# Kernel tuning notes

Hardware: AMD Instinct MI355X
Metric: run time of the kernel (lower is better)

## Reference

```python
import jax, jax.numpy as jnp
import numpy as np

FEATURES = [3, 64, 128, 256]
N_ITER = 5  # NNMF multiplicative-update iterations
K = 3
PAD = K // 2  # 'same' padding so spatial dims are preserved inside a block
EPS = 1e-20
BN_EPS = 1e-5


def conv2d(x, w, pad):
    # x: [B, Cin, H, W], w: [Cout, Cin, kh, kw] (torch OIHW layout)
    return jax.lax.conv_general_dilated(
        x, w, window_strides=(1, 1),
        padding=[(pad, pad), (pad, pad)],
        dimension_numbers=("NCHW", "OIHW", "NCHW"))


def nnmf_conv2d(x, w, n_iter, pad):
    # Non-negative, L1-normalized weights (per output filter)
    wp = jnp.abs(w)
    wn = wp / (wp.sum(axis=(1, 2, 3), keepdims=True) + EPS)
    # Input is non-negative (ReLU applied upstream); L1-normalize over channels
    x = x / (x.sum(axis=1, keepdims=True) + EPS)
    b, _, hh, ww = x.shape
    c_out = w.shape[0]
    # h init: uniform distribution over output channels
    h = jnp.full((b, c_out, hh, ww), 1.0 / c_out, dtype=x.dtype)
    # conv_transpose2d(h, W, padding=pad) == conv2d(h, flip(W).swap(O,I), padding=k-1-pad);
    # with odd k and pad = k//2 this is again 'same' padding.
    wt = jnp.transpose(jnp.flip(wn, (2, 3)), (1, 0, 2, 3))  # [Cin, Cout, kh, kw] as OIHW
    for _ in range(n_iter):
        recon = conv2d(h, wt, pad)                    # [B, Cin, H, W]
        h = h * conv2d(x / (recon + EPS), wn, pad)    # multiplicative update
        h = h / (h.sum(axis=1, keepdims=True) + EPS)  # renormalize over channels
    return h


def batchnorm(x, gamma, beta):
    # Training-mode BN: batch statistics over (N, H, W), biased variance
    mean = x.mean(axis=(0, 2, 3), keepdims=True)
    var = x.var(axis=(0, 2, 3), keepdims=True)
    xn = (x - mean) * jax.lax.rsqrt(var + BN_EPS)
    return xn * gamma[None, :, None, None] + beta[None, :, None, None]


def avgpool2(x):
    b, c, h, w = x.shape
    return x.reshape(b, c, h // 2, 2, w // 2, 2).mean(axis=(3, 5))


def block(x, w_nnmf, w_conv, b_conv, gamma, beta):
    x = jax.nn.relu(x)
    h = nnmf_conv2d(x, w_nnmf, N_ITER, PAD)
    y = conv2d(h, w_conv, 0) + b_conv[None, :, None, None]  # 1x1 conv
    y = jax.nn.relu(y)
    y = batchnorm(y, gamma, beta)
    return avgpool2(y)


def setup_inputs() -> dict:
    key = jax.random.key(0)
    keys = jax.random.split(key, 7)
    inp = {"x": jax.random.normal(keys[0], (16, 3, 128, 128), jnp.float32)}
    for i in range(3):
        cin, cout = FEATURES[i], FEATURES[i + 1]
        inp[f"w_nnmf{i}"] = jax.random.uniform(keys[1 + 2 * i], (cout, cin, K, K), jnp.float32)
        inp[f"w_conv{i}"] = jax.random.normal(keys[2 + 2 * i], (cout, cout, 1, 1), jnp.float32) / np.sqrt(cout).astype(np.float32)
        inp[f"b_conv{i}"] = jnp.zeros((cout,), jnp.float32)
        inp[f"gamma{i}"] = jnp.ones((cout,), jnp.float32)
        inp[f"beta{i}"] = jnp.zeros((cout,), jnp.float32)
    return inp


def reference(x, w_nnmf0, w_conv0, b_conv0, gamma0, beta0,
              w_nnmf1, w_conv1, b_conv1, gamma1, beta1,
              w_nnmf2, w_conv2, b_conv2, gamma2, beta2):
    x = block(x, w_nnmf0, w_conv0, b_conv0, gamma0, beta0)
    x = block(x, w_nnmf1, w_conv1, b_conv1, gamma1, beta1)
    x = block(x, w_nnmf2, w_conv2, b_conv2, gamma2, beta2)
    return x  # [16, 256, 16, 16]
```

## Files before the change

kernel.cpp:

```cpp
#include <hip/hip_runtime.h>

#define EPSV  1e-20f
#define BNEPS 1e-5f

typedef _Float16 f16x8 __attribute__((ext_vector_type(8)));
typedef _Float16 f16x4 __attribute__((ext_vector_type(4)));
typedef float    f32x4 __attribute__((ext_vector_type(4)));

__device__ inline unsigned pack2f16(float a, float b) {
    unsigned short ua = __builtin_bit_cast(unsigned short, (_Float16)a);
    unsigned short ub = __builtin_bit_cast(unsigned short, (_Float16)b);
    return ((unsigned)ub << 16) | ua;
}

template<int CIN, int COUT>
__global__ __launch_bounds__(256) void prep_w_f16_kernel(const float* __restrict__ w,
                                                         _Float16* __restrict__ wAh,
                                                         _Float16* __restrict__ wBh)
{
    const int co  = blockIdx.x;
    const int tid = threadIdx.x;
    const int N   = CIN * 9;
    const float* wrow = w + (size_t)co * N;

    float s = 0.f;
    for (int i = tid; i < N; i += 256) s += fabsf(wrow[i]);
    __shared__ float red[4];
    #pragma unroll
    for (int m = 32; m; m >>= 1) s += __shfl_xor(s, m, 64);
    if ((tid & 63) == 0) red[tid >> 6] = s;
    __syncthreads();
    s = red[0] + red[1] + red[2] + red[3];
    const float rn = 1.f / (s + EPSV);

    for (int i = tid; i < N; i += 256) {
        const int ci = i / 9, tap = i % 9;
        const int ky = tap / 3, kx = tap % 3;
        const float v = fabsf(wrow[i]) * rn;
        const int tf = (2 - ky) * 3 + (2 - kx);
        wBh[(((size_t)(ci >> 5) * 9 + tap) * COUT + co) * 32 + (ci & 31)] = (_Float16)v;
        wAh[(((size_t)(co >> 5) * 9 + tf) * CIN + ci) * 32 + (co & 31)] = (_Float16)v;
    }
}

__global__ __launch_bounds__(256) void zero_f16_kernel(_Float16* __restrict__ a, int n)
{
    const int i = blockIdx.x * 256 + threadIdx.x;
    if (i < n) a[i] = (_Float16)0.f;
}

__global__ __launch_bounds__(64) void prep_w0_kernel(const float* __restrict__ w,
                                                     _Float16* __restrict__ wA0h,
                                                     _Float16* __restrict__ wB0h)
{
    const int co = blockIdx.x, tid = threadIdx.x;
    float s = (tid < 27) ? fabsf(w[co * 27 + tid]) : 0.f;
    #pragma unroll
    for (int m = 32; m; m >>= 1) s += __shfl_xor(s, m, 64);
    const float rn = 1.f / (s + EPSV);
    if (tid < 27) {
        const int ci = tid / 9, tap = tid % 9, ky = tap / 3, kx = tap % 3;
        const float v = fabsf(w[co * 27 + tid]) * rn;
        const int tf = (2 - ky) * 3 + (2 - kx);
        wB0h[co * 64 + tap * 4 + ci] = (_Float16)v;
        wA0h[(((co >> 5) * 9 + tf) * 16 + ci) * 32 + (co & 31)] = (_Float16)v;
    }
}

__global__ __launch_bounds__(256) void prep_w1h_kernel(const float* __restrict__ w1,
                                                       _Float16* __restrict__ w1h, int n)
{
    const int i = blockIdx.x * 256 + threadIdx.x;
    if (i < n) w1h[i] = (_Float16)w1[i];
}

__global__ __launch_bounds__(256) void xn0_kernel(const float* __restrict__ x,
                                                  _Float16* __restrict__ xn4,
                                                  int npx, int HW)
{
    const int p = blockIdx.x * 256 + threadIdx.x;
    if (p >= npx) return;
    const int b = p / HW, r = p % HW;
    const float* ip = x + (size_t)b * 3 * HW + r;
    const float v0 = fmaxf(ip[0], 0.f), v1 = fmaxf(ip[HW], 0.f), v2 = fmaxf(ip[2 * HW], 0.f);
    const float rs = 1.f / (v0 + v1 + v2 + EPSV);
    unsigned* d = (unsigned*)(xn4 + (size_t)p * 4);
    d[0] = pack2f16(v0 * rs, v1 * rs);
    d[1] = pack2f16(v2 * rs, 0.f);
}

template<int C>
__global__ __launch_bounds__(256) void xn12_kernel(const _Float16* __restrict__ prev,
                                                   _Float16* __restrict__ xn, int npx)
{
    const int p = blockIdx.x * 256 + threadIdx.x;
    if (p >= npx) return;
    const _Float16* ip = prev + (size_t)p * C;
    _Float16* op = xn + (size_t)p * C;
    f16x8 buf[C / 8];
    float s = 0.f;
    #pragma unroll
    for (int g = 0; g < C / 8; ++g) {
        buf[g] = *(const f16x8*)(ip + g * 8);
        #pragma unroll
        for (int j = 0; j < 8; ++j) {
            float v = fmaxf((float)buf[g][j], 0.f);
            s += v;
            buf[g][j] = (_Float16)v;
        }
    }
    const float rs = 1.f / (s + EPSV);
    #pragma unroll
    for (int g = 0; g < C / 8; ++g) {
        f16x8 o;
        #pragma unroll
        for (int j = 0; j < 8; ++j) o[j] = (_Float16)((float)buf[g][j] * rs);
        *(f16x8*)(op + g * 8) = o;
    }
}

__global__ __launch_bounds__(256) void init_h_kernel(_Float16* __restrict__ h, float* __restrict__ S,
                                                     int nh, int ns, float cval)
{
    const int i = blockIdx.x * 256 + threadIdx.x;
    if (i < nh) h[i] = (_Float16)1.f;
    if (i < ns) S[i] = cval;
}

template<int NS>
__global__ __launch_bounds__(256) void combine_S_kernel(const float* __restrict__ sp,
                                                        float* __restrict__ S, int npx)
{
    const int i = blockIdx.x * 256 + threadIdx.x;
    if (i >= npx) return;
    float s = sp[i];
    #pragma unroll
    for (int k = 1; k < NS; ++k) s += sp[(size_t)k * npx + i];
    S[i] = s;
}

template<int ICg, int OCg, int NSPLIT, int OST, int NW, bool NORM_IN, bool UPDATE>
__global__ __launch_bounds__(256, 1) void mfconv5(
    const _Float16* __restrict__ in, const _Float16* __restrict__ wgt,
    const _Float16* __restrict__ aux, _Float16* __restrict__ out,
    const float* __restrict__ Sin, float* __restrict__ Sout,
    int H, int W, int sstride)
{
    constexpr int OCWG = OCg / NSPLIT;
    constexpr int NF = OCWG / 16;
    constexpr int HS = 18, WSp = 18, NSP = HS * WSp;
    constexpr int ICP = 40;
    constexpr int NCH = ICg / 32;
    constexpr int LS = (NSPLIT == 4) ? 2 : (NSPLIT == 2) ? 1 : 0;
    constexpr int NLD = NSP * 4;
    constexpr int IREG = (NLD + 255) / 256;
    constexpr int WOC = OCWG * 32;
    constexpr int NWLD = 9 * OCWG * 4;
    constexpr int WREG = (NWLD + 255) / 256;
    static_assert(OCWG % 16 == 0 && ICg % 32 == 0, "cfg");

    __shared__ _Float16 in_t[2][NSP * ICP];
    __shared__ _Float16 w_t[2][9 * WOC];
    __shared__ float rS[NORM_IN ? NSP : 1];

    const int tid = threadIdx.x;
    const int lane = tid & 63, wave = tid >> 6;
    const int kq = lane >> 4, l15 = lane & 15;
    const int split = blockIdx.x & (NSPLIT - 1);
    const int tx = blockIdx.x >> LS;
    const int x0 = tx * 16, y0 = blockIdx.y * 16, b = blockIdx.z;
    const int HW = H * W;
    const int oc0 = split * OCWG;

    f16x8 ild[IREG];
    f16x8 wld[WREG];

    auto iload = [&](int kc) {
        #pragma unroll
        for (int r = 0; r < IREG; ++r) {
            const int i = tid + r * 256;
            f16x8 v = {0, 0, 0, 0, 0, 0, 0, 0};
            if (i < NLD) {
                const int sp = i >> 2, seg = i & 3;
                const int yy = y0 + sp / WSp - 1, xx = x0 + sp % WSp - 1;
                if (yy >= 0 && yy < H && xx >= 0 && xx < W)
                    v = __builtin_nontemporal_load((const f16x8*)(in +
                        ((size_t)b * HW + (size_t)yy * W + xx) * ICg + kc * 32 + seg * 8));
            }
            ild[r] = v;
        }
    };
    auto wload = [&](int kc) {
        #pragma unroll
        for (int r = 0; r < WREG; ++r) {
            const int j = tid + r * 256;
            if (j < NWLD) {
                const int tap = j / (OCWG * 4), rem = j % (OCWG * 4);
                const int oc = rem >> 2, e = rem & 3;
                wld[r] = *(const f16x8*)(wgt +
                    (((size_t)kc * 9 + tap) * OCg + oc0 + oc) * 32 + e * 8);
            }
        }
    };
    auto iwrite = [&](int buf) {
        #pragma unroll
        for (int r = 0; r < IREG; ++r) {
            const int i = tid + r * 256;
            if (i < NLD) {
                const int sp = i >> 2, seg = i & 3;
                if constexpr (NORM_IN) {
                    const float f = rS[sp];
                    unsigned* d = (unsigned*)&in_t[buf][sp * ICP + seg * 8];
                    d[0] = pack2f16((float)ild[r][0] * f, (float)ild[r][1] * f);
                    d[1] = pack2f16((float)ild[r][2] * f, (float)ild[r][3] * f);
                    d[2] = pack2f16((float)ild[r][4] * f, (float)ild[r][5] * f);
                    d[3] = pack2f16((float)ild[r][6] * f, (float)ild[r][7] * f);
                } else {
                    *(f16x8*)&in_t[buf][sp * ICP + seg * 8] = ild[r];
                }
            }
        }
    };
    auto wwrite = [&](int buf) {
        #pragma unroll
        for (int r = 0; r < WREG; ++r) {
            const int j = tid + r * 256;
            if (j < NWLD) {
                const int tap = j / (OCWG * 4), rem = j % (OCWG * 4);
                const int oc = rem >> 2, e = rem & 3;
                const int slot = e ^ ((oc >> 1) & 3);
                *(f16x8*)&w_t[buf][tap * WOC + oc * 32 + slot * 8] = wld[r];
            }
        }
    };

    const int prow = wave * 4;

    f32x4 acc[4][NF];
    #pragma unroll
    for (int mf = 0; mf < 4; ++mf)
        #pragma unroll
        for (int nf = 0; nf < NF; ++nf) acc[mf][nf] = (f32x4){0.f, 0.f, 0.f, 0.f};

    iload(0); wload(0);
    if constexpr (NORM_IN) {
        for (int i = tid; i < NSP; i += 256) {
            const int yy = y0 + i / WSp - 1, xx = x0 + i % WSp - 1;
            float sv = 0.f;
            if (yy >= 0 && yy < H && xx >= 0 && xx < W)
                sv = Sin[(size_t)b * HW + (size_t)yy * W + xx];
            rS[i] = 1.f / (sv + EPSV);
        }
        __syncthreads();
    }
    iwrite(0); wwrite(0);
    __syncthreads();

    int cur = 0;
    for (int kc = 0; kc < NCH; ++kc) {
        if (kc + 1 < NCH) { iload(kc + 1); wload(kc + 1); }
        {
            const _Float16* ib = &in_t[cur][0];
            const _Float16* wb = &w_t[cur][0];
            #pragma unroll
            for (int dy = 0; dy < 3; ++dy) {
                #pragma unroll
                for (int dx = 0; dx < 3; ++dx) {
                    const int tap = dy * 3 + dx;
                    f16x8 bfr[NF];
                    #pragma unroll
                    for (int nf = 0; nf < NF; ++nf) {
                        const int oc = nf * 16 + l15;
                        bfr[nf] = *(const f16x8*)(
                            wb + tap * WOC + oc * 32 + (kq ^ ((oc >> 1) & 3)) * 8);
                    }
                    f16x8 afr[4];
                    #pragma unroll
                    for (int mf = 0; mf < 4; ++mf)
                        afr[mf] = *(const f16x8*)(
                            ib + ((prow + mf + dy) * WSp + l15 + dx) * ICP + kq * 8);
                    #pragma unroll
                    for (int mf = 0; mf < 4; ++mf)
                        #pragma unroll
                        for (int nf = 0; nf < NF; ++nf)
                            acc[mf][nf] = __builtin_amdgcn_mfma_f32_16x16x32_f16(
                                afr[mf], bfr[nf], acc[mf][nf], 0, 0, 0);
                }
            }
        }
        if (kc + 1 < NCH) {
            iwrite(cur ^ 1); wwrite(cur ^ 1);
            __syncthreads();
            cur ^= 1;
        }
    }

    #pragma unroll
    for (int mf = 0; mf < 4; ++mf) {
        const int gy = y0 + prow + mf;
        const size_t pixbase = (size_t)b * HW + (size_t)gy * W + x0 + kq * 4;
        if constexpr (!UPDATE) {
            #pragma unroll
            for (int nf = 0; nf < NF; ++nf) {
                const int oc = oc0 + nf * 16 + l15;
                if (oc < NW) {
                    #pragma unroll
                    for (int r = 0; r < 4; ++r) {
                        const size_t idx = (pixbase + r) * OST + oc;
                        out[idx] = (_Float16)((float)aux[idx] / (acc[mf][nf][r] + EPSV));
                    }
                }
            }
        } else {
            float s[4] = {0.f, 0.f, 0.f, 0.f};
            #pragma unroll
            for (int nf = 0; nf < NF; ++nf) {
                const int oc = oc0 + nf * 16 + l15;
                #pragma unroll
                for (int r = 0; r < 4; ++r) {
                    const size_t idx = (pixbase + r) * OST + oc;
                    const float hv = (float)out[idx] * acc[mf][nf][r];
                    const _Float16 hq = (_Float16)hv;
                    out[idx] = hq;
                    s[r] += (float)hq;
                }
            }
            #pragma unroll
            for (int mm = 1; mm < 16; mm <<= 1) {
                #pragma unroll
                for (int r = 0; r < 4; ++r) s[r] += __shfl_xor(s[r], mm);
            }
            if (l15 == 0) {
                float* sp_ = Sout + (size_t)split * sstride + pixbase;
                sp_[0] = s[0]; sp_[1] = s[1]; sp_[2] = s[2]; sp_[3] = s[3];
            }
        }
    }
}

__global__ __launch_bounds__(256) void mf0u_kernel(
    const _Float16* __restrict__ ratio4, const _Float16* __restrict__ wB0h,
    _Float16* __restrict__ h, float* __restrict__ Sout, int H, int W)
{
    constexpr int TW = 16;
    __shared__ _Float16 a_t[64 * 72];

    const int tid = threadIdx.x;
    const int lane = tid & 63, wave = tid >> 6;
    const int kq = lane >> 4, l15 = lane & 15;
    const int x0 = blockIdx.x * TW, y0 = blockIdx.y * 4, b = blockIdx.z;
    const int HW = H * W;

    for (int i = tid; i < 64 * 72 / 2; i += 256) ((unsigned*)a_t)[i] = 0;
    __syncthreads();
    for (int i = tid; i < 576; i += 256) {
        const int px = i / 9, tap = i % 9;
        const int py = px / TW, pxx = px % TW;
        const int yy = y0 + py + tap / 3 - 1, xx = x0 + pxx + tap % 3 - 1;
        if (yy >= 0 && yy < H && xx >= 0 && xx < W)
            *(f16x4*)&a_t[px * 72 + tap * 4] =
                *(const f16x4*)(ratio4 + ((size_t)b * HW + (size_t)yy * W + xx) * 4);
    }
    __syncthreads();

    f32x4 acc[4];
    #pragma unroll
    for (int nf = 0; nf < 4; ++nf) acc[nf] = (f32x4){0.f, 0.f, 0.f, 0.f};
    #pragma unroll
    for (int kc = 0; kc < 2; ++kc) {
        const f16x8 afr = *(const f16x8*)&a_t[(wave * 16 + l15) * 72 + kc * 32 + kq * 8];
        #pragma unroll
        for (int nf = 0; nf < 4; ++nf) {
            const f16x8 bfr = *(const f16x8*)(wB0h + (size_t)(nf * 16 + l15) * 64 + kc * 32 + kq * 8);
            acc[nf] = __builtin_amdgcn_mfma_f32_16x16x32_f16(afr, bfr, acc[nf], 0, 0, 0);
        }
    }

    const int pl = wave * 16 + kq * 4;
    const size_t pixbase = (size_t)b * HW + (size_t)(y0 + pl / TW) * W + x0 + pl % TW;
    float s[4] = {0.f, 0.f, 0.f, 0.f};
    #pragma unroll
    for (int nf = 0; nf < 4; ++nf) {
        const int oc = nf * 16 + l15;
        #pragma unroll
        for (int r = 0; r < 4; ++r) {
            const size_t idx = (pixbase + r) * 64 + oc;
            const float hv = (float)h[idx] * acc[nf][r];
            const _Float16 hq = (_Float16)hv;
            h[idx] = hq;
            s[r] += (float)hq;
        }
    }
    #pragma unroll
    for (int mm = 1; mm < 16; mm <<= 1) {
        #pragma unroll
        for (int r = 0; r < 4; ++r) s[r] += __shfl_xor(s[r], mm);
    }
    if (l15 == 0) {
        float* sp_ = Sout + pixbase;
        sp_[0] = s[0]; sp_[1] = s[1]; sp_[2] = s[2]; sp_[3] = s[3];
    }
}

template<int C, int MODE>
__global__ __launch_bounds__(256) void posty_kernel(
    const _Float16* __restrict__ h, const float* __restrict__ S,
    const _Float16* __restrict__ w1h, const float* __restrict__ bias,
    const float* __restrict__ bnst, float* __restrict__ part,
    void* __restrict__ outp, int H, int W)
{
    constexpr int NF = C / 16, CP = C + 8;
    __shared__ _Float16 a_t[64 * CP];
    __shared__ float rs_t[64];
    __shared__ float sred1[MODE == 0 ? 4 * C : 1];
    __shared__ float sred2[MODE == 0 ? 4 * C : 1];

    const int tid = threadIdx.x;
    const int lane = tid & 63, wave = tid >> 6;
    const int kq = lane >> 4, l15 = lane & 15;
    const int WT = W / 32;
    const int tx = blockIdx.x % WT, ty = blockIdx.x / WT;
    const int b = blockIdx.y;
    const int HW = H * W;

    if (tid < 64) {
        const int gp = (2 * ty + (tid >> 5)) * W + tx * 32 + (tid & 31);
        rs_t[tid] = 1.f / (S[(size_t)b * HW + gp] + EPSV);
    }
    __syncthreads();
    for (int i = tid; i < 64 * (C / 8); i += 256) {
        const int sp = i / (C / 8), seg = i % (C / 8);
        const int gp = (2 * ty + (sp >> 5)) * W + tx * 32 + (sp & 31);
        const f16x8 v = *(const f16x8*)(h + ((size_t)b * HW + gp) * C + seg * 8);
        const float f = rs_t[sp];
        unsigned* d = (unsigned*)&a_t[sp * CP + seg * 8];
        d[0] = pack2f16((float)v[0] * f, (float)v[1] * f);
        d[1] = pack2f16((float)v[2] * f, (float)v[3] * f);
        d[2] = pack2f16((float)v[4] * f, (float)v[5] * f);
        d[3] = pack2f16((float)v[6] * f, (float)v[7] * f);
    }
    __syncthreads();

    f32x4 acc[NF];
    #pragma unroll
    for (int nf = 0; nf < NF; ++nf) acc[nf] = (f32x4){0.f, 0.f, 0.f, 0.f};
    #pragma unroll
    for (int kc = 0; kc < C / 32; ++kc) {
        const f16x8 afr = *(const f16x8*)&a_t[(wave * 16 + l15) * CP + kc * 32 + kq * 8];
        #pragma unroll
        for (int nf = 0; nf < NF; ++nf) {
            const f16x8 bfr = *(const f16x8*)(w1h + (size_t)(nf * 16 + l15) * C + kc * 32 + kq * 8);
            acc[nf] = __builtin_amdgcn_mfma_f32_16x16x32_f16(afr, bfr, acc[nf], 0, 0, 0);
        }
    }

    const int pl = wave * 16 + kq * 4;

    if constexpr (MODE == 0) {
        const int wgid = b * gridDim.x + blockIdx.x;
        #pragma unroll
        for (int nf = 0; nf < NF; ++nf) {
            const int oc = nf * 16 + l15;
            const float bv = bias[oc];
            float s1 = 0.f, s2 = 0.f;
            #pragma unroll
            for (int r = 0; r < 4; ++r) {
                const float y = fmaxf(acc[nf][r] + bv, 0.f);
                s1 += y; s2 += y * y;
            }
            s1 += __shfl_xor(s1, 16); s2 += __shfl_xor(s2, 16);
            s1 += __shfl_xor(s1, 32); s2 += __shfl_xor(s2, 32);
            if (kq == 0) {
                sred1[wave * C + oc] = s1;
                sred2[wave * C + oc] = s2;
            }
        }
        __syncthreads();
        for (int oc = tid; oc < C; oc += 256) {
            const float s1 = sred1[oc] + sred1[C + oc] + sred1[2 * C + oc] + sred1[3 * C + oc];
            const float s2 = sred2[oc] + sred2[C + oc] + sred2[2 * C + oc] + sred2[3 * C + oc];
            part[((size_t)wgid * C + oc) * 2 + 0] = s1;
            part[((size_t)wgid * C + oc) * 2 + 1] = s2;
        }
    } else {
        __syncthreads();
        #pragma unroll
        for (int nf = 0; nf < NF; ++nf) {
            const int oc = nf * 16 + l15;
            const float bv = bias[oc];
            #pragma unroll
            for (int r = 0; r < 4; ++r)
                a_t[(pl + r) * CP + oc] = (_Float16)fmaxf(acc[nf][r] + bv, 0.f);
        }
        __syncthreads();
        const int Wo = W >> 1;
        for (int i = tid; i < 16 * C; i += 256) {
            int ox, c;
            if constexpr (MODE == 1) { c = i % C; ox = i / C; }
            else                     { ox = i % 16; c = i / 16; }
            const float y00 = (float)a_t[(2 * ox) * CP + c];
            const float y01 = (float)a_t[(2 * ox + 1) * CP + c];
            const float y10 = (float)a_t[(32 + 2 * ox) * CP + c];
            const float y11 = (float)a_t[(32 + 2 * ox + 1) * CP + c];
            const float v = (y00 + y01 + y10 + y11) * 0.25f * bnst[c] + bnst[C + c];
            if constexpr (MODE == 1) {
                ((_Float16*)outp)[((size_t)b * (HW >> 2) + (size_t)ty * Wo + tx * 16 + ox) * C + c] =
                    (_Float16)v;
            } else {
                ((float*)outp)[(((size_t)b * C + c) * (size_t)(H >> 1) + ty) * Wo + tx * 16 + ox] = v;
            }
        }
    }
}

template<int C>
__global__ __launch_bounds__(256) void stats_kernel(const float* __restrict__ part, int nwg, float invM,
                                                    const float* __restrict__ gamma,
                                                    const float* __restrict__ beta,
                                                    float* __restrict__ stats)
{
    const int oc = blockIdx.x;
    const int tid = threadIdx.x;
    float s1 = 0.f, s2 = 0.f;
    for (int w = tid; w < nwg; w += 256) {
        s1 += part[((size_t)w * C + oc) * 2 + 0];
        s2 += part[((size_t)w * C + oc) * 2 + 1];
    }
    __shared__ float r1[4], r2[4];
    #pragma unroll
    for (int m = 32; m; m >>= 1) { s1 += __shfl_xor(s1, m, 64); s2 += __shfl_xor(s2, m, 64); }
    if ((tid & 63) == 0) { r1[tid >> 6] = s1; r2[tid >> 6] = s2; }
    __syncthreads();
    if (tid == 0) {
        s1 = r1[0] + r1[1] + r1[2] + r1[3];
        s2 = r2[0] + r2[1] + r2[2] + r2[3];
        const float mean = s1 * invM;
        const float var  = s2 * invM - mean * mean;
        const float rstd = rsqrtf(var + BNEPS);
        const float scale = gamma[oc] * rstd;
        stats[oc]     = scale;
        stats[C + oc] = beta[oc] - mean * scale;
    }
}

extern "C" void kernel_launch(void* const* d_in, const int* in_sizes, int n_in,
                              void* d_out, int out_size, void* d_ws, size_t ws_size,
                              hipStream_t stream)
{
    const float* x = (const float*)d_in[0];
    float* ws      = (float*)d_ws;
    float* S       = ws;
    float* part    = S + 262144;
    float* bnstats = part + 1048576;
    _Float16* h      = (_Float16*)(bnstats + 512);
    _Float16* xnh    = h + 16777216;
    _Float16* ratioh = xnh + 4194304;
    _Float16* out0h  = ratioh + 4194304;
    _Float16* out1h  = out0h + 4194304;
    _Float16* wAh    = out1h + 2097152;
    _Float16* wBh    = wAh + 294912;
    _Float16* w1h    = wBh + 294912;
    _Float16* wA0h   = w1h + 65536;
    _Float16* wB0h   = wA0h + 9216;

    const int B = 16;

    {
        const int H = 128, W = 128, HW = H * W, npx = B * HW;
        zero_f16_kernel<<<(9216 + 255) / 256, 256, 0, stream>>>(wA0h, 9216);
        prep_w0_kernel<<<64, 64, 0, stream>>>((const float*)d_in[1], wA0h, wB0h);
        xn0_kernel<<<npx / 256, 256, 0, stream>>>(x, xnh, npx, HW);
        init_h_kernel<<<(npx * 64 + 255) / 256, 256, 0, stream>>>(h, S, npx * 64, npx, 64.f);
        for (int it = 0; it < 5; ++it) {
            mfconv5<64, 16, 1, 4, 4, true, false>
                <<<dim3(8, 8, B), 256, 0, stream>>>(h, wA0h, xnh, ratioh, S, nullptr, H, W, 0);
            mf0u_kernel<<<dim3(8, 32, B), 256, 0, stream>>>(ratioh, wB0h, h, S, H, W);
        }
        prep_w1h_kernel<<<16, 256, 0, stream>>>((const float*)d_in[2], w1h, 64 * 64);
        dim3 pg((W / 32) * (H / 2), B);
        posty_kernel<64, 0><<<pg, 256, 0, stream>>>(h, S, w1h, (const float*)d_in[3],
                                                    nullptr, part, nullptr, H, W);
        stats_kernel<64><<<64, 256, 0, stream>>>(part, pg.x * pg.y, 1.0f / (float)npx,
                                                 (const float*)d_in[4], (const float*)d_in[5], bnstats);
        posty_kernel<64, 1><<<pg, 256, 0, stream>>>(h, S, w1h, (const float*)d_in[3],
                                                    bnstats, nullptr, out0h, H, W);
    }

    {
        const int H = 64, W = 64, HW = H * W, npx = B * HW;
        prep_w_f16_kernel<64, 128><<<128, 256, 0, stream>>>((const float*)d_in[6], wAh, wBh);
        xn12_kernel<64><<<npx / 256, 256, 0, stream>>>(out0h, xnh, npx);
        init_h_kernel<<<(npx * 128 + 255) / 256, 256, 0, stream>>>(h, S, npx * 128, npx, 128.f);
        for (int it = 0; it < 5; ++it) {
            mfconv5<128, 64, 1, 64, 64, true, false>
                <<<dim3(4, 4, B), 256, 0, stream>>>(h, wAh, xnh, ratioh, S, nullptr, H, W, 0);
            mfconv5<64, 128, 2, 128, 128, false, true>
                <<<dim3(8, 4, B), 256, 0, stream>>>(ratioh, wBh, nullptr, h, nullptr, part, H, W, npx);
            combine_S_kernel<2><<<(npx + 255) / 256, 256, 0, stream>>>(part, S, npx);
        }
        prep_w1h_kernel<<<64, 256, 0, stream>>>((const float*)d_in[7], w1h, 128 * 128);
        dim3 pg((W / 32) * (H / 2), B);
        posty_kernel<128, 0><<<pg, 256, 0, stream>>>(h, S, w1h, (const float*)d_in[8],
                                                     nullptr, part, nullptr, H, W);
        stats_kernel<128><<<128, 256, 0, stream>>>(part, pg.x * pg.y, 1.0f / (float)npx,
                                                   (const float*)d_in[9], (const float*)d_in[10], bnstats);
        posty_kernel<128, 1><<<pg, 256, 0, stream>>>(h, S, w1h, (const float*)d_in[8],
                                                     bnstats, nullptr, out1h, H, W);
    }

    {
        const int H = 32, W = 32, HW = H * W, npx = B * HW;
        prep_w_f16_kernel<128, 256><<<256, 256, 0, stream>>>((const float*)d_in[11], wAh, wBh);
        xn12_kernel<128><<<npx / 256, 256, 0, stream>>>(out1h, xnh, npx);
        init_h_kernel<<<(npx * 256 + 255) / 256, 256, 0, stream>>>(h, S, npx * 256, npx, 256.f);
        for (int it = 0; it < 5; ++it) {
            mfconv5<256, 128, 2, 128, 128, true, false>
                <<<dim3(4, 2, B), 256, 0, stream>>>(h, wAh, xnh, ratioh, S, nullptr, H, W, 0);
            mfconv5<128, 256, 4, 256, 256, false, true>
                <<<dim3(8, 2, B), 256, 0, stream>>>(ratioh, wBh, nullptr, h, nullptr, part, H, W, npx);
            combine_S_kernel<4><<<(npx + 255) / 256, 256, 0, stream>>>(part, S, npx);
        }
        prep_w1h_kernel<<<256, 256, 0, stream>>>((const float*)d_in[12], w1h, 256 * 256);
        dim3 pg((W / 32) * (H / 2), B);
        posty_kernel<256, 0><<<pg, 256, 0, stream>>>(h, S, w1h, (const float*)d_in[13],
                                                     nullptr, part, nullptr, H, W);
        stats_kernel<256><<<256, 256, 0, stream>>>(part, pg.x * pg.y, 1.0f / (float)npx,
                                                   (const float*)d_in[14], (const float*)d_in[15], bnstats);
        posty_kernel<256, 2><<<pg, 256, 0, stream>>>(h, S, w1h, (const float*)d_in[13],
                                                     bnstats, nullptr, d_out, H, W);
    }
}
```

Baseline: 958.6 us.

## Specialize first NNMF iteration, fuse input normalization and S-partial combine into consumers

Several small kernels are removed. The first iteration of each block gets a FIRST specialization that treats h as a known constant: the input tile is filled with 1/C and no h is read for the multiplicative update, which drops init_h. The partial channel sums S are no longer merged by combine_S; consumers sum the NSIN partials directly. The ReLU+L1 normalization (xn12) moves into the pooling epilogue of posty, which writes straight into the next block's xn buffer. The block-2 A-pass split changes from 2 to 4. This cuts launches and memory passes, at the cost of more template variants and extra reductions inside the posty epilogue.

```diff
diff --git a/kernel.cpp b/kernel.cpp
--- a/kernel.cpp
+++ b/kernel.cpp
@@ -89,63 +89,15 @@
     d[1] = pack2f16(v2 * rs, 0.f);
 }
 
-template<int C>
-__global__ __launch_bounds__(256) void xn12_kernel(const _Float16* __restrict__ prev,
-                                                   _Float16* __restrict__ xn, int npx)
-{
-    const int p = blockIdx.x * 256 + threadIdx.x;
-    if (p >= npx) return;
-    const _Float16* ip = prev + (size_t)p * C;
-    _Float16* op = xn + (size_t)p * C;
-    f16x8 buf[C / 8];
-    float s = 0.f;
-    #pragma unroll
-    for (int g = 0; g < C / 8; ++g) {
-        buf[g] = *(const f16x8*)(ip + g * 8);
-        #pragma unroll
-        for (int j = 0; j < 8; ++j) {
-            float v = fmaxf((float)buf[g][j], 0.f);
-            s += v;
-            buf[g][j] = (_Float16)v;
-        }
-    }
-    const float rs = 1.f / (s + EPSV);
-    #pragma unroll
-    for (int g = 0; g < C / 8; ++g) {
-        f16x8 o;
-        #pragma unroll
-        for (int j = 0; j < 8; ++j) o[j] = (_Float16)((float)buf[g][j] * rs);
-        *(f16x8*)(op + g * 8) = o;
-    }
-}
-
-__global__ __launch_bounds__(256) void init_h_kernel(_Float16* __restrict__ h, float* __restrict__ S,
-                                                     int nh, int ns, float cval)
-{
-    const int i = blockIdx.x * 256 + threadIdx.x;
-    if (i < nh) h[i] = (_Float16)1.f;
-    if (i < ns) S[i] = cval;
-}
-
-template<int NS>
-__global__ __launch_bounds__(256) void combine_S_kernel(const float* __restrict__ sp,
-                                                        float* __restrict__ S, int npx)
-{
-    const int i = blockIdx.x * 256 + threadIdx.x;
-    if (i >= npx) return;
-    float s = sp[i];
-    #pragma unroll
-    for (int k = 1; k < NS; ++k) s += sp[(size_t)k * npx + i];
-    S[i] = s;
-}
-
-template<int ICg, int OCg, int NSPLIT, int OST, int NW, bool NORM_IN, bool UPDATE>
+template<int ICg, int OCg, int NSPLIT, int OST, int NW, int NSIN,
+         bool NORM_IN, bool UPDATE, bool FIRST>
 __global__ __launch_bounds__(256, 1) void mfconv5(
     const _Float16* __restrict__ in, const _Float16* __restrict__ wgt,
     const _Float16* __restrict__ aux, _Float16* __restrict__ out,
     const float* __restrict__ Sin, float* __restrict__ Sout,
     int H, int W, int sstride)
 {
+    constexpr bool CSTAGE = FIRST && NORM_IN;
     constexpr int OCWG = OCg / NSPLIT;
     constexpr int NF = OCWG / 16;
     constexpr int HS = 18, WSp = 18, NSP = HS * WSp;
@@ -159,9 +111,9 @@
     constexpr int WREG = (NWLD + 255) / 256;
     static_assert(OCWG % 16 == 0 && ICg % 32 == 0, "cfg");
 
-    __shared__ _Float16 in_t[2][NSP * ICP];
+    __shared__ _Float16 in_t[CSTAGE ? 1 : 2][NSP * ICP];
     __shared__ _Float16 w_t[2][9 * WOC];
-    __shared__ float rS[NORM_IN ? NSP : 1];
+    __shared__ float rS[(NORM_IN && !FIRST) ? NSP : 1];
 
     const int tid = threadIdx.x;
     const int lane = tid & 63, wave = tid >> 6;
@@ -172,7 +124,7 @@
     const int HW = H * W;
     const int oc0 = split * OCWG;
 
-    f16x8 ild[IREG];
+    f16x8 ild[CSTAGE ? 1 : IREG];
     f16x8 wld[WREG];
 
     auto iload = [&](int kc) {
@@ -208,7 +160,7 @@
             const int i = tid + r * 256;
             if (i < NLD) {
                 const int sp = i >> 2, seg = i & 3;
-                if constexpr (NORM_IN) {
+                if constexpr (NORM_IN && !FIRST) {
                     const float f = rS[sp];
                     unsigned* d = (unsigned*)&in_t[buf][sp * ICP + seg * 8];
                     d[0] = pack2f16((float)ild[r][0] * f, (float)ild[r][1] * f);
@@ -242,25 +194,44 @@
         #pragma unroll
         for (int nf = 0; nf < NF; ++nf) acc[mf][nf] = (f32x4){0.f, 0.f, 0.f, 0.f};
 
-    iload(0); wload(0);
-    if constexpr (NORM_IN) {
+    if constexpr (!CSTAGE) iload(0);
+    wload(0);
+    if constexpr (NORM_IN && !FIRST) {
         for (int i = tid; i < NSP; i += 256) {
             const int yy = y0 + i / WSp - 1, xx = x0 + i % WSp - 1;
             float sv = 0.f;
-            if (yy >= 0 && yy < H && xx >= 0 && xx < W)
-                sv = Sin[(size_t)b * HW + (size_t)yy * W + xx];
+            if (yy >= 0 && yy < H && xx >= 0 && xx < W) {
+                const size_t pix = (size_t)b * HW + (size_t)yy * W + xx;
+                #pragma unroll
+                for (int k = 0; k < NSIN; ++k) sv += Sin[(size_t)k * sstride + pix];
+            }
             rS[i] = 1.f / (sv + EPSV);
         }
         __syncthreads();
     }
-    iwrite(0); wwrite(0);
+    if constexpr (CSTAGE) {
+        const unsigned cpk = pack2f16(1.0f / (float)ICg, 1.0f / (float)ICg);
+        for (int i = tid; i < NSP; i += 256) {
+            const int yy = y0 + i / WSp - 1, xx = x0 + i % WSp - 1;
+            const bool ok = (yy >= 0 && yy < H && xx >= 0 && xx < W);
+            unsigned* d = (unsigned*)&in_t[0][i * ICP];
+            #pragma unroll
+            for (int seg = 0; seg < 16; ++seg) d[seg] = ok ? cpk : 0u;
+        }
+    } else {
+        iwrite(0);
+    }
+    wwrite(0);
     __syncthreads();
 
     int cur = 0;
     for (int kc = 0; kc < NCH; ++kc) {
-        if (kc + 1 < NCH) { iload(kc + 1); wload(kc + 1); }
+        if (kc + 1 < NCH) {
+            if constexpr (!CSTAGE) iload(kc + 1);
+            wload(kc + 1);
+        }
         {
-            const _Float16* ib = &in_t[cur][0];
+            const _Float16* ib = &in_t[CSTAGE ? 0 : cur][0];
             const _Float16* wb = &w_t[cur][0];
             #pragma unroll
             for (int dy = 0; dy < 3; ++dy) {
@@ -289,7 +260,8 @@
             }
         }
         if (kc + 1 < NCH) {
-            iwrite(cur ^ 1); wwrite(cur ^ 1);
+            if constexpr (!CSTAGE) iwrite(cur ^ 1);
+            wwrite(cur ^ 1);
             __syncthreads();
             cur ^= 1;
         }
@@ -319,7 +291,9 @@
                 #pragma unroll
                 for (int r = 0; r < 4; ++r) {
                     const size_t idx = (pixbase + r) * OST + oc;
-                    const float hv = (float)out[idx] * acc[mf][nf][r];
+                    float hv;
+                    if constexpr (FIRST) hv = acc[mf][nf][r];
+                    else                 hv = (float)out[idx] * acc[mf][nf][r];
                     const _Float16 hq = (_Float16)hv;
                     out[idx] = hq;
                     s[r] += (float)hq;
@@ -338,6 +312,7 @@
     }
 }
 
+template<bool FIRST>
 __global__ __launch_bounds__(256) void mf0u_kernel(
     const _Float16* __restrict__ ratio4, const _Float16* __restrict__ wB0h,
     _Float16* __restrict__ h, float* __restrict__ Sout, int H, int W)
@@ -385,7 +360,9 @@
         #pragma unroll
         for (int r = 0; r < 4; ++r) {
             const size_t idx = (pixbase + r) * 64 + oc;
-            const float hv = (float)h[idx] * acc[nf][r];
+            float hv;
+            if constexpr (FIRST) hv = acc[nf][r];
+            else                 hv = (float)h[idx] * acc[nf][r];
             const _Float16 hq = (_Float16)hv;
             h[idx] = hq;
             s[r] += (float)hq;
@@ -402,18 +379,19 @@
     }
 }
 
-template<int C, int MODE>
+template<int C, int MODE, int NSIN>
 __global__ __launch_bounds__(256) void posty_kernel(
     const _Float16* __restrict__ h, const float* __restrict__ S,
     const _Float16* __restrict__ w1h, const float* __restrict__ bias,
     const float* __restrict__ bnst, float* __restrict__ part,
-    void* __restrict__ outp, int H, int W)
+    void* __restrict__ outp, int H, int W, int sst)
 {
     constexpr int NF = C / 16, CP = C + 8;
     __shared__ _Float16 a_t[64 * CP];
     __shared__ float rs_t[64];
     __shared__ float sred1[MODE == 0 ? 4 * C : 1];
     __shared__ float sred2[MODE == 0 ? 4 * C : 1];
+    __shared__ float pool_t[MODE == 1 ? 16 * (C + 1) : 1];
 
     const int tid = threadIdx.x;
     const int lane = tid & 63, wave = tid >> 6;
@@ -425,7 +403,10 @@
 
     if (tid < 64) {
         const int gp = (2 * ty + (tid >> 5)) * W + tx * 32 + (tid & 31);
-        rs_t[tid] = 1.f / (S[(size_t)b * HW + gp] + EPSV);
+        float sv = 0.f;
+        #pragma unroll
+        for (int k = 0; k < NSIN; ++k) sv += S[(size_t)k * sst + (size_t)b * HW + gp];
+        rs_t[tid] = 1.f / (sv + EPSV);
     }
     __syncthreads();
     for (int i = tid; i < 64 * (C / 8); i += 256) {
@@ -494,21 +475,37 @@
         }
         __syncthreads();
         const int Wo = W >> 1;
-        for (int i = tid; i < 16 * C; i += 256) {
-            int ox, c;
-            if constexpr (MODE == 1) { c = i % C; ox = i / C; }
-            else                     { ox = i % 16; c = i / 16; }
-            const float y00 = (float)a_t[(2 * ox) * CP + c];
-            const float y01 = (float)a_t[(2 * ox + 1) * CP + c];
-            const float y10 = (float)a_t[(32 + 2 * ox) * CP + c];
-            const float y11 = (float)a_t[(32 + 2 * ox + 1) * CP + c];
-            const float v = (y00 + y01 + y10 + y11) * 0.25f * bnst[c] + bnst[C + c];
-            if constexpr (MODE == 1) {
-                ((_Float16*)outp)[((size_t)b * (HW >> 2) + (size_t)ty * Wo + tx * 16 + ox) * C + c] =
-                    (_Float16)v;
-            } else {
+        if constexpr (MODE == 2) {
+            for (int i = tid; i < 16 * C; i += 256) {
+                const int ox = i % 16, c = i / 16;
+                const float y00 = (float)a_t[(2 * ox) * CP + c];
+                const float y01 = (float)a_t[(2 * ox + 1) * CP + c];
+                const float y10 = (float)a_t[(32 + 2 * ox) * CP + c];
+                const float y11 = (float)a_t[(32 + 2 * ox + 1) * CP + c];
+                const float v = (y00 + y01 + y10 + y11) * 0.25f * bnst[c] + bnst[C + c];
                 ((float*)outp)[(((size_t)b * C + c) * (size_t)(H >> 1) + ty) * Wo + tx * 16 + ox] = v;
             }
+        } else {
+            for (int i = tid; i < 16 * C; i += 256) {
+                const int ox = i / C, c = i % C;
+                const float y00 = (float)a_t[(2 * ox) * CP + c];
+                const float y01 = (float)a_t[(2 * ox + 1) * CP + c];
+                const float y10 = (float)a_t[(32 + 2 * ox) * CP + c];
+                const float y11 = (float)a_t[(32 + 2 * ox + 1) * CP + c];
+                pool_t[ox * (C + 1) + c] =
+                    fmaxf((y00 + y01 + y10 + y11) * 0.25f * bnst[c] + bnst[C + c], 0.f);
+            }
+            __syncthreads();
+            const int px = tid >> 4, prt = tid & 15;
+            float ps = 0.f;
+            for (int c = prt; c < C; c += 16) ps += pool_t[px * (C + 1) + c];
+            ps += __shfl_xor(ps, 1); ps += __shfl_xor(ps, 2);
+            ps += __shfl_xor(ps, 4); ps += __shfl_xor(ps, 8);
+            const float rs = 1.f / (ps + EPSV);
+            _Float16* xo = (_Float16*)outp;
+            const size_t obase = ((size_t)b * (HW >> 2) + (size_t)ty * Wo + tx * 16 + px) * C;
+            for (int c = prt; c < C; c += 16)
+                xo[obase + c] = (_Float16)(pool_t[px * (C + 1) + c] * rs);
         }
     }
 }
@@ -555,9 +552,7 @@
     _Float16* h      = (_Float16*)(bnstats + 512);
     _Float16* xnh    = h + 16777216;
     _Float16* ratioh = xnh + 4194304;
-    _Float16* out0h  = ratioh + 4194304;
-    _Float16* out1h  = out0h + 4194304;
-    _Float16* wAh    = out1h + 2097152;
+    _Float16* wAh    = ratioh + 4194304;
     _Float16* wBh    = wAh + 294912;
     _Float16* w1h    = wBh + 294912;
     _Float16* wA0h   = w1h + 65536;
@@ -570,63 +565,67 @@
         zero_f16_kernel<<<(9216 + 255) / 256, 256, 0, stream>>>(wA0h, 9216);
         prep_w0_kernel<<<64, 64, 0, stream>>>((const float*)d_in[1], wA0h, wB0h);
         xn0_kernel<<<npx / 256, 256, 0, stream>>>(x, xnh, npx, HW);
-        init_h_kernel<<<(npx * 64 + 255) / 256, 256, 0, stream>>>(h, S, npx * 64, npx, 64.f);
-        for (int it = 0; it < 5; ++it) {
-            mfconv5<64, 16, 1, 4, 4, true, false>
-                <<<dim3(8, 8, B), 256, 0, stream>>>(h, wA0h, xnh, ratioh, S, nullptr, H, W, 0);
-            mf0u_kernel<<<dim3(8, 32, B), 256, 0, stream>>>(ratioh, wB0h, h, S, H, W);
+        mfconv5<64, 16, 1, 4, 4, 1, true, false, true>
+            <<<dim3(8, 8, B), 256, 0, stream>>>(h, wA0h, xnh, ratioh, S, nullptr, H, W, npx);
+        mf0u_kernel<true><<<dim3(8, 32, B), 256, 0, stream>>>(ratioh, wB0h, h, S, H, W);
+        for (int it = 1; it < 5; ++it) {
+            mfconv5<64, 16, 1, 4, 4, 1, true, false, false>
+                <<<dim3(8, 8, B), 256, 0, stream>>>(h, wA0h, xnh, ratioh, S, nullptr, H, W, npx);
+            mf0u_kernel<false><<<dim3(8, 32, B), 256, 0, stream>>>(ratioh, wB0h, h, S, H, W);
         }
         prep_w1h_kernel<<<16, 256, 0, stream>>>((const float*)d_in[2], w1h, 64 * 64);
         dim3 pg((W / 32) * (H / 2), B);
-        posty_kernel<64, 0><<<pg, 256, 0, stream>>>(h, S, w1h, (const float*)d_in[3],
-                                                    nullptr, part, nullptr, H, W);
+        posty_kernel<64, 0, 1><<<pg, 256, 0, stream>>>(h, S, w1h, (const float*)d_in[3],
+                                                       nullptr, part, nullptr, H, W, npx);
         stats_kernel<64><<<64, 256, 0, stream>>>(part, pg.x * pg.y, 1.0f / (float)npx,
                                                  (const float*)d_in[4], (const float*)d_in[5], bnstats);
-        posty_kernel<64, 1><<<pg, 256, 0, stream>>>(h, S, w1h, (const float*)d_in[3],
-                                                    bnstats, nullptr, out0h, H, W);
+        posty_kernel<64, 1, 1><<<pg, 256, 0, stream>>>(h, S, w1h, (const float*)d_in[3],
+                                                       bnstats, nullptr, xnh, H, W, npx);
     }
 
     {
         const int H = 64, W = 64, HW = H * W, npx = B * HW;
         prep_w_f16_kernel<64, 128><<<128, 256, 0, stream>>>((const float*)d_in[6], wAh, wBh);
-        xn12_kernel<64><<<npx / 256, 256, 0, stream>>>(out0h, xnh, npx);
-        init_h_kernel<<<(npx * 128 + 255) / 256, 256, 0, stream>>>(h, S, npx * 128, npx, 128.f);
-        for (int it = 0; it < 5; ++it) {
-            mfconv5<128, 64, 1, 64, 64, true, false>
-                <<<dim3(4, 4, B), 256, 0, stream>>>(h, wAh, xnh, ratioh, S, nullptr, H, W, 0);
-            mfconv5<64, 128, 2, 128, 128, false, true>
-                <<<dim3(8, 4, B), 256, 0, stream>>>(ratioh, wBh, nullptr, h, nullptr, part, H, W, npx);
-            combine_S_kernel<2><<<(npx + 255) / 256, 256, 0, stream>>>(part, S, npx);
+        mfconv5<128, 64, 1, 64, 64, 1, true, false, true>
+            <<<dim3(4, 4, B), 256, 0, stream>>>(h, wAh, xnh, ratioh, S, nullptr, H, W, npx);
+        mfconv5<64, 128, 2, 128, 128, 1, false, true, true>
+            <<<dim3(8, 4, B), 256, 0, stream>>>(ratioh, wBh, nullptr, h, nullptr, S, H, W, npx);
+        for (int it = 1; it < 5; ++it) {
+            mfconv5<128, 64, 1, 64, 64, 2, true, false, false>
+                <<<dim3(4, 4, B), 256, 0, stream>>>(h, wAh, xnh, ratioh, S, nullptr, H, W, npx);
+            mfconv5<64, 128, 2, 128, 128, 1, false, true, false>
+                <<<dim3(8, 4, B), 256, 0, stream>>>(ratioh, wBh, nullptr, h, nullptr, S, H, W, npx);
         }
         prep_w1h_kernel<<<64, 256, 0, stream>>>((const float*)d_in[7], w1h, 128 * 128);
         dim3 pg((W / 32) * (H / 2), B);
-        posty_kernel<128, 0><<<pg, 256, 0, stream>>>(h, S, w1h, (const float*)d_in[8],
-                                                     nullptr, part, nullptr, H, W);
+        posty_kernel<128, 0, 2><<<pg, 256, 0, stream>>>(h, S, w1h, (const float*)d_in[8],
+                                                        nullptr, part, nullptr, H, W, npx);
         stats_kernel<128><<<128, 256, 0, stream>>>(part, pg.x * pg.y, 1.0f / (float)npx,
                                                    (const float*)d_in[9], (const float*)d_in[10], bnstats);
-        posty_kernel<128, 1><<<pg, 256, 0, stream>>>(h, S, w1h, (const float*)d_in[8],
-                                                     bnstats, nullptr, out1h, H, W);
+        posty_kernel<128, 1, 2><<<pg, 256, 0, stream>>>(h, S, w1h, (const float*)d_in[8],
+                                                        bnstats, nullptr, xnh, H, W, npx);
     }
 
     {
         const int H = 32, W = 32, HW = H * W, npx = B * HW;
         prep_w_f16_kernel<128, 256><<<256, 256, 0, stream>>>((const float*)d_in[11], wAh, wBh);
-        xn12_kernel<128><<<npx / 256, 256, 0, stream>>>(out1h, xnh, npx);
-        init_h_kernel<<<(npx * 256 + 255) / 256, 256, 0, stream>>>(h, S, npx * 256, npx, 256.f);
-        for (int it = 0; it < 5; ++it) {
-            mfconv5<256, 128, 2, 128, 128, true, false>
-                <<<dim3(4, 2, B), 256, 0, stream>>>(h, wAh, xnh, ratioh, S, nullptr, H, W, 0);
-            mfconv5<128, 256, 4, 256, 256, false, true>
-                <<<dim3(8, 2, B), 256, 0, stream>>>(ratioh, wBh, nullptr, h, nullptr, part, H, W, npx);
-            combine_S_kernel<4><<<(npx + 255) / 256, 256, 0, stream>>>(part, S, npx);
+        mfconv5<256, 128, 4, 128, 128, 1, true, false, true>
+            <<<dim3(8, 2, B), 256, 0, stream>>>(h, wAh, xnh, ratioh, S, nullptr, H, W, npx);
+        mfconv5<128, 256, 4, 256, 256, 1, false, true, true>
+            <<<dim3(8, 2, B), 256, 0, stream>>>(ratioh, wBh, nullptr, h, nullptr, S, H, W, npx);
+        for (int it = 1; it < 5; ++it) {
+            mfconv5<256, 128, 4, 128, 128, 4, true, false, false>
+                <<<dim3(8, 2, B), 256, 0, stream>>>(h, wAh, xnh, ratioh, S, nullptr, H, W, npx);
+            mfconv5<128, 256, 4, 256, 256, 1, false, true, false>
+                <<<dim3(8, 2, B), 256, 0, stream>>>(ratioh, wBh, nullptr, h, nullptr, S, H, W, npx);
         }
         prep_w1h_kernel<<<256, 256, 0, stream>>>((const float*)d_in[12], w1h, 256 * 256);
         dim3 pg((W / 32) * (H / 2), B);
-        posty_kernel<256, 0><<<pg, 256, 0, stream>>>(h, S, w1h, (const float*)d_in[13],
-                                                     nullptr, part, nullptr, H, W);
+        posty_kernel<256, 0, 4><<<pg, 256, 0, stream>>>(h, S, w1h, (const float*)d_in[13],
+                                                        nullptr, part, nullptr, H, W, npx);
         stats_kernel<256><<<256, 256, 0, stream>>>(part, pg.x * pg.y, 1.0f / (float)npx,
                                                    (const float*)d_in[14], (const float*)d_in[15], bnstats);
-        posty_kernel<256, 2><<<pg, 256, 0, stream>>>(h, S, w1h, (const float*)d_in[13],
-                                                     bnstats, nullptr, d_out, H, W);
-    }
-}
+        posty_kernel<256, 2, 4><<<pg, 256, 0, stream>>>(h, S, w1h, (const float*)d_in[13],
+                                                        bnstats, nullptr, d_out, H, W, npx);
+    }
+}
```

After: 824.7 us. 1.16x faster.
